# Kernel tuning notes

Measured on AMD Instinct MI355X. Metric: run time of the kernel, lower is better.

The kernel has to match this reference:

```python
import jax, jax.numpy as jnp
import numpy as np
import math

N = 100000          # nodes
E = 3200000         # edges
F_IN = 500          # num_features
HID = 64            # hidden
C = 64              # num_classes
K = 5               # trig frequencies
OMEGA = 1.0
D = 10              # Taylor order / diffusion hops


def _taylor_coeffs():
    # cos/sin Taylor coefficient tables, [K, D+1] (static, fp64 then cast)
    x = (np.arange(1, K + 1) * OMEGA * np.pi)[:, None].astype(np.float64)
    cosc = np.zeros((K, D + 1), np.float64)
    sinc = np.zeros((K, D + 1), np.float64)
    even = np.arange(0, D + 1, 2)
    cosc[:, ::2] = ((-1.0) ** (even // 2)) * x ** even / np.array([math.factorial(int(o)) for o in even], np.float64)
    odd = np.arange(1, D + 1, 2)
    sinc[:, 1::2] = ((-1.0) ** ((odd - 1) // 2)) * x ** odd / np.array([math.factorial(int(o)) for o in odd], np.float64)
    return jnp.asarray(sinc, jnp.float32), jnp.asarray(cosc, jnp.float32)

SINC, COSC = _taylor_coeffs()


def setup_inputs() -> dict:
    key = jax.random.key(0)
    ks = jax.random.split(key, 8)
    feature = jax.random.normal(ks[0], (N, F_IN), dtype=jnp.float32)
    edges = jax.random.randint(ks[1], (2, E), 0, N, dtype=jnp.int64)
    W1 = jax.random.normal(ks[2], (F_IN, HID), dtype=jnp.float32) * (1.0 / np.sqrt(F_IN))
    b1 = jnp.zeros((HID,), jnp.float32)
    W2 = jax.random.normal(ks[3], (HID, C), dtype=jnp.float32) * (1.0 / np.sqrt(HID))
    b2 = jnp.zeros((C,), jnp.float32)
    xav = np.sqrt(2.0 / (1 + K))  # xavier_normal for (1, K)
    alpha = jax.random.normal(ks[4], (1, K), dtype=jnp.float32) * xav
    beta = jax.random.normal(ks[5], (1, K), dtype=jnp.float32) * xav
    return {"feature": feature, "edges": edges, "W1": W1, "b1": b1,
            "W2": W2, "b2": b2, "alpha": alpha, "beta": beta}


def reference(feature, edges, W1, b1, W2, b2, alpha, beta):
    # dropout is identity in eval mode
    x = jnp.maximum(feature @ W1 + b1, 0.0)   # lin1 + relu
    x = x @ W2 + b2                           # lin2 -> [N, C]

    # ---- Trigo_prop.__norm__: sym-normalized Laplacian, rescale, self-loops -1 ----
    src, dst = edges[0], edges[1]
    not_loop = src != dst                     # remove_self_loops
    deg = jax.ops.segment_sum(jnp.where(not_loop, 1.0, 0.0).astype(x.dtype), src, num_segments=N)
    dinv = jnp.where(deg > 0, jax.lax.rsqrt(deg), 0.0)
    w_off = jnp.where(not_loop, -(dinv[src] * dinv[dst]), 0.0)   # off-diag of L_sym
    # Laplacian diagonal entries are all 1 -> lambda_max = 2*max(all weights)
    lam = 2.0 * jnp.maximum(jnp.max(w_off), 1.0)
    s = 2.0 / lam
    w_off = w_off * s
    diag = s * 1.0 - 1.0                      # scaled diag(1) plus appended -1 self-loop

    # ---- D-hop Taylor-weighted diffusion ----
    coeff = (alpha @ SINC + beta @ COSC)[0]   # [D+1]
    Tx = x
    hidden = coeff[0] * Tx
    for d in range(1, D + 1):                 # fixed small D, unrolled
        Tx = jax.ops.segment_sum(w_off[:, None] * Tx[src], dst, num_segments=N) + diag * Tx
        hidden = hidden + coeff[d] * Tx
    out = hidden + x
    return jax.nn.log_softmax(out, axis=1)
```

## Files before the change

### kernel.cpp

```cpp
#include <hip/hip_runtime.h>
#include <math.h>

#define NN 100000
#define FIN 500
#define HIDN 64
#define KF 5
#define DORD 10

typedef unsigned short ushort_t;

struct Tables { float sinc[KF][DORD+1]; float cosc[KF][DORD+1]; };

__device__ inline float bl(unsigned u) { return __uint_as_float(u << 16); }
__device__ inline float bh(unsigned u) { return __uint_as_float(u & 0xffff0000u); }
__device__ inline unsigned short bf16_rne(float x) {
    unsigned u = __float_as_uint(x);
    return (unsigned short)((u + 0x7fffu + ((u >> 16) & 1u)) >> 16);
}
__device__ inline unsigned pack_bf16x2(float a, float b) {
    return (unsigned)bf16_rne(a) | ((unsigned)bf16_rne(b) << 16);
}

__global__ void coeff_kernel(const float* __restrict__ alpha, const float* __restrict__ beta,
                             Tables tb, float* __restrict__ coeff) {
    int d = threadIdx.x;
    if (d <= DORD) {
        float c = 0.f;
        #pragma unroll
        for (int k = 0; k < KF; ++k)
            c += alpha[k] * tb.sinc[k][d] + beta[k] * tb.cosc[k][d];
        coeff[d] = c;
    }
}

#define CHUNK 8192
__global__ __launch_bounds__(256) void bin_hist_kernel(
    const int* __restrict__ src, const int* __restrict__ dst,
    int* __restrict__ deg, int* __restrict__ bucket_cnt,
    int E, int drng, int nb) {
    __shared__ int h[512];
    for (int i = threadIdx.x; i < nb; i += 256) h[i] = 0;
    __syncthreads();
    int base = blockIdx.x * CHUNK;
    int end = base + CHUNK; if (end > E) end = E;
    for (int e = base + threadIdx.x; e < end; e += 256) {
        int s = src[e], d = dst[e];
        if (s != d) {
            atomicAdd(&deg[s], 1);
            atomicAdd(&h[d / drng], 1);
        }
    }
    __syncthreads();
    for (int i = threadIdx.x; i < nb; i += 256)
        if (h[i]) atomicAdd(&bucket_cnt[i], h[i]);
}

__global__ void dinv_kernel(const int* __restrict__ deg, float* __restrict__ dinv, int n) {
    int i = blockIdx.x * blockDim.x + threadIdx.x;
    if (i >= n) return;
    int d = deg[i];
    dinv[i] = (d > 0) ? (1.0f / sqrtf((float)d)) : 0.f;
}

__global__ void bucket_scan_kernel(const int* __restrict__ bucket_cnt,
                                   int* __restrict__ bucket_off,
                                   int* __restrict__ bucket_cur, int nb) {
    __shared__ int tmp[512];
    int t = threadIdx.x;
    tmp[t] = (t < nb) ? bucket_cnt[t] : 0;
    __syncthreads();
    for (int off = 1; off < 512; off <<= 1) {
        int add = (t >= off) ? tmp[t - off] : 0;
        __syncthreads();
        tmp[t] += add;
        __syncthreads();
    }
    int excl = (t > 0) ? tmp[t - 1] : 0;
    if (t < nb) { bucket_off[t] = excl; bucket_cur[t] = excl; }
    if (t == nb - 1) bucket_off[nb] = tmp[t];
}

__global__ __launch_bounds__(256) void bin_scatter_kernel(
    const int* __restrict__ src, const int* __restrict__ dst,
    int* __restrict__ bucket_cur, uint2* __restrict__ binned,
    int E, int drng, int nb) {
    __shared__ int h[512];
    for (int i = threadIdx.x; i < nb; i += 256) h[i] = 0;
    __syncthreads();
    int base = blockIdx.x * CHUNK;
    int end = base + CHUNK; if (end > E) end = E;
    for (int e = base + threadIdx.x; e < end; e += 256) {
        int s = src[e], d = dst[e];
        if (s != d) atomicAdd(&h[d / drng], 1);
    }
    __syncthreads();
    for (int i = threadIdx.x; i < nb; i += 256) {
        int c = h[i];
        h[i] = c ? atomicAdd(&bucket_cur[i], c) : 0;
    }
    __syncthreads();
    for (int e = base + threadIdx.x; e < end; e += 256) {
        int s = src[e], d = dst[e];
        if (s != d) {
            int pos = atomicAdd(&h[d / drng], 1);
            binned[pos] = make_uint2((unsigned)s, (unsigned)d);
        }
    }
}

__global__ __launch_bounds__(256) void bucket_csr_kernel(
    const uint2* __restrict__ binned, const int* __restrict__ bucket_off,
    int* __restrict__ row_ptr, int* __restrict__ col,
    int n, int drng, int nb) {
    int b = blockIdx.x;
    int e0 = bucket_off[b], e1 = bucket_off[b + 1];
    int d0 = b * drng;
    int dn = n - d0; if (dn > drng) dn = drng;
    __shared__ int ind[256];
    __shared__ int cur[256];
    int t = threadIdx.x;
    ind[t] = 0;
    __syncthreads();
    for (int e = e0 + t; e < e1; e += 256) {
        uint2 p = binned[e];
        atomicAdd(&ind[(int)p.y - d0], 1);
    }
    __syncthreads();
    for (int off = 1; off < 256; off <<= 1) {
        int add = (t >= off) ? ind[t - off] : 0;
        __syncthreads();
        ind[t] += add;
        __syncthreads();
    }
    if (t < dn) {
        int excl = (t > 0) ? ind[t - 1] : 0;
        row_ptr[d0 + t] = e0 + excl;
        cur[t] = e0 + excl;
    }
    if (b == 0 && t == 0) row_ptr[n] = bucket_off[nb];
    __syncthreads();
    for (int e = e0 + t; e < e1; e += 256) {
        uint2 p = binned[e];
        int pos = atomicAdd(&cur[(int)p.y - d0], 1);
        col[pos] = (int)p.x;
    }
}

__global__ __launch_bounds__(256) void gemm1_kernel(
    const float* __restrict__ A, const float* __restrict__ W,
    const float* __restrict__ bias, float* __restrict__ H, int n) {
    __shared__ float sA[64][36];
    __shared__ float sW[32][64];
    int t = threadIdx.x;
    int tx = t & 15, ty = t >> 4;
    int rowBase = blockIdx.x * 64;
    float acc[4][4] = {{0.f}};
    for (int k0 = 0; k0 < FIN; k0 += 32) {
        #pragma unroll
        for (int l = 0; l < 2; ++l) {
            int c = t + l * 256;
            int r = c >> 3, cc = (c & 7) * 4;
            int gr = rowBase + r, gk = k0 + cc;
            float4 v = make_float4(0.f, 0.f, 0.f, 0.f);
            if (gr < n && gk < FIN) v = *(const float4*)(A + (size_t)gr * FIN + gk);
            *(float4*)&sA[r][cc] = v;
        }
        #pragma unroll
        for (int l = 0; l < 2; ++l) {
            int c = t + l * 256;
            int r = c >> 4, cc = (c & 15) * 4;
            int gk = k0 + r;
            float4 v = make_float4(0.f, 0.f, 0.f, 0.f);
            if (gk < FIN) v = *(const float4*)(W + (size_t)gk * 64 + cc);
            *(float4*)&sW[r][cc] = v;
        }
        __syncthreads();
        #pragma unroll
        for (int kk = 0; kk < 32; ++kk) {
            float a[4], b[4];
            #pragma unroll
            for (int i = 0; i < 4; ++i) a[i] = sA[ty * 4 + i][kk];
            #pragma unroll
            for (int j = 0; j < 4; ++j) b[j] = sW[kk][tx * 4 + j];
            #pragma unroll
            for (int i = 0; i < 4; ++i)
                #pragma unroll
                for (int j = 0; j < 4; ++j)
                    acc[i][j] = fmaf(a[i], b[j], acc[i][j]);
        }
        __syncthreads();
    }
    #pragma unroll
    for (int i = 0; i < 4; ++i) {
        int gr = rowBase + ty * 4 + i;
        if (gr < n) {
            float4 o;
            o.x = fmaxf(acc[i][0] + bias[tx * 4 + 0], 0.f);
            o.y = fmaxf(acc[i][1] + bias[tx * 4 + 1], 0.f);
            o.z = fmaxf(acc[i][2] + bias[tx * 4 + 2], 0.f);
            o.w = fmaxf(acc[i][3] + bias[tx * 4 + 3], 0.f);
            *(float4*)(H + (size_t)gr * 64 + tx * 4) = o;
        }
    }
}

__global__ __launch_bounds__(256) void gemm2_kernel(
    const float* __restrict__ H, const float* __restrict__ W2,
    const float* __restrict__ b2, const float* __restrict__ coeff,
    const float* __restrict__ dinv, ushort_t* __restrict__ ty0,
    float* __restrict__ out, int n) {
    __shared__ float sW[64 * 64];
    __shared__ float sb[64];
    int t = threadIdx.x;
    for (int i = t; i < 4096; i += 256) sW[i] = W2[i];
    if (t < 64) sb[t] = b2[t];
    __syncthreads();
    float c0p1 = 1.f + coeff[0];
    int lane = t & 63;
    int wid = t >> 6;
    int r0 = blockIdx.x * 128;
    int rend = r0 + 128; if (rend > n) rend = n;
    for (int r = r0 + wid; r < rend; r += 4) {
        float hv = H[(size_t)r * 64 + lane];
        float dr = dinv[r];
        float acc = sb[lane];
        #pragma unroll
        for (int k = 0; k < 64; ++k)
            acc = fmaf(__shfl(hv, k, 64), sW[k * 64 + lane], acc);
        ty0[(size_t)r * 64 + lane] = bf16_rne(dr * acc);
        out[(size_t)r * 64 + lane] = c0p1 * acc;
    }
}

__global__ __launch_bounds__(256) void spmm_kernel(
    const int* __restrict__ row_ptr, const int* __restrict__ col,
    const float* __restrict__ dinv, const ushort_t* __restrict__ tyin,
    ushort_t* __restrict__ tyout, float* __restrict__ out,
    const float* __restrict__ coeff, int d, int n, int fuse_lsm) {
    int wave = (blockIdx.x * blockDim.x + threadIdx.x) >> 6;
    if (wave >= n) return;
    int lane = threadIdx.x & 63;
    int sub = lane >> 4;
    int fl = lane & 15;
    int e0 = row_ptr[wave], e1 = row_ptr[wave + 1];
    float ax = 0.f, ay = 0.f, az = 0.f, aw = 0.f;
    int e = e0 + sub;
    for (; e + 12 < e1; e += 16) {
        int s0 = col[e], s1 = col[e + 4], s2 = col[e + 8], s3 = col[e + 12];
        uint2 p0 = *(const uint2*)(tyin + (size_t)s0 * 64 + fl * 4);
        uint2 p1 = *(const uint2*)(tyin + (size_t)s1 * 64 + fl * 4);
        uint2 p2 = *(const uint2*)(tyin + (size_t)s2 * 64 + fl * 4);
        uint2 p3 = *(const uint2*)(tyin + (size_t)s3 * 64 + fl * 4);
        ax += (bl(p0.x) + bl(p1.x)) + (bl(p2.x) + bl(p3.x));
        ay += (bh(p0.x) + bh(p1.x)) + (bh(p2.x) + bh(p3.x));
        az += (bl(p0.y) + bl(p1.y)) + (bl(p2.y) + bl(p3.y));
        aw += (bh(p0.y) + bh(p1.y)) + (bh(p2.y) + bh(p3.y));
    }
    for (; e < e1; e += 4) {
        int s = col[e];
        uint2 p = *(const uint2*)(tyin + (size_t)s * 64 + fl * 4);
        ax += bl(p.x); ay += bh(p.x); az += bl(p.y); aw += bh(p.y);
    }
    #pragma unroll
    for (int off = 16; off <= 32; off <<= 1) {
        ax += __shfl_xor(ax, off, 64);
        ay += __shfl_xor(ay, off, 64);
        az += __shfl_xor(az, off, 64);
        aw += __shfl_xor(aw, off, 64);
    }
    float dr = dinv[wave];
    float cd = coeff[d];
    float tx_x = -dr * ax, tx_y = -dr * ay, tx_z = -dr * az, tx_w = -dr * aw;
    float4 o = *(const float4*)(out + (size_t)wave * 64 + fl * 4);
    o.x += cd * tx_x; o.y += cd * tx_y; o.z += cd * tx_z; o.w += cd * tx_w;
    if (!fuse_lsm) {
        if (sub == 0) {
            uint2 ty;
            ty.x = pack_bf16x2(dr * tx_x, dr * tx_y);
            ty.y = pack_bf16x2(dr * tx_z, dr * tx_w);
            *(uint2*)(tyout + (size_t)wave * 64 + fl * 4) = ty;
            *(float4*)(out + (size_t)wave * 64 + fl * 4) = o;
        }
    } else {
        float m = fmaxf(fmaxf(o.x, o.y), fmaxf(o.z, o.w));
        #pragma unroll
        for (int off = 1; off < 16; off <<= 1) m = fmaxf(m, __shfl_xor(m, off, 64));
        float s4 = expf(o.x - m) + expf(o.y - m) + expf(o.z - m) + expf(o.w - m);
        #pragma unroll
        for (int off = 1; off < 16; off <<= 1) s4 += __shfl_xor(s4, off, 64);
        float lse = m + logf(s4);
        o.x -= lse; o.y -= lse; o.z -= lse; o.w -= lse;
        if (sub == 0)
            *(float4*)(out + (size_t)wave * 64 + fl * 4) = o;
    }
}

extern "C" void kernel_launch(void* const* d_in, const int* in_sizes, int n_in,
                              void* d_out, int out_size, void* d_ws, size_t ws_size,
                              hipStream_t stream) {
    const float* feature = (const float*)d_in[0];
    const int*   edges   = (const int*)d_in[1];
    const float* W1      = (const float*)d_in[2];
    const float* b1      = (const float*)d_in[3];
    const float* W2      = (const float*)d_in[4];
    const float* b2      = (const float*)d_in[5];
    const float* alpha   = (const float*)d_in[6];
    const float* beta    = (const float*)d_in[7];
    float* out = (float*)d_out;

    const int n = in_sizes[0] / FIN;
    const int E = in_sizes[1] / 2;
    const int* src = edges;
    const int* dst = edges + E;

    const int drng = (n + 511) / 512;
    const int nb   = (n + drng - 1) / drng;

    char* ws = (char*)d_ws;
    size_t off = 0;
    auto alloc = [&](size_t bytes) { size_t o = off; off = (off + bytes + 255) & ~(size_t)255; return o; };
    float*    coeff      = (float*)   (ws + alloc(64 * 4));
    int*      deg        = (int*)     (ws + alloc((size_t)n * 4));
    float*    dinv       = (float*)   (ws + alloc((size_t)n * 4));
    int*      row_ptr    = (int*)     (ws + alloc(((size_t)n + 1) * 4));
    int*      bucket_cnt = (int*)     (ws + alloc(512 * 4));
    int*      bucket_off = (int*)     (ws + alloc(513 * 4));
    int*      bucket_cur = (int*)     (ws + alloc(512 * 4));
    int*      col        = (int*)     (ws + alloc((size_t)E * 4));
    uint2*    binned     = (uint2*)   (ws + alloc((size_t)E * 8));
    float*    H          = (float*)   (ws + alloc((size_t)n * 64 * 4));
    ushort_t* TyA        = (ushort_t*)(ws + alloc((size_t)n * 64 * 2));
    ushort_t* TyB        = (ushort_t*)(ws + alloc((size_t)n * 64 * 2));

    Tables tb;
    for (int k = 0; k < KF; ++k) {
        double x = M_PI * (double)(k + 1);
        double p = 1.0, f = 1.0;
        for (int o = 0; o <= DORD; ++o) {
            if (o > 0) { p *= x; f *= (double)o; }
            double v = p / f;
            tb.cosc[k][o] = (o % 2 == 0) ? (float)((((o / 2) % 2 == 0) ? 1.0 : -1.0) * v) : 0.f;
            tb.sinc[k][o] = (o % 2 == 1) ? (float)(((((o - 1) / 2) % 2 == 0) ? 1.0 : -1.0) * v) : 0.f;
        }
    }

    hipMemsetAsync(deg, 0, (size_t)n * 4, stream);
    hipMemsetAsync(bucket_cnt, 0, 512 * 4, stream);

    coeff_kernel<<<1, 64, 0, stream>>>(alpha, beta, tb, coeff);

    int nchunk = (E + CHUNK - 1) / CHUNK;
    bin_hist_kernel<<<nchunk, 256, 0, stream>>>(src, dst, deg, bucket_cnt, E, drng, nb);
    dinv_kernel<<<(n + 255) / 256, 256, 0, stream>>>(deg, dinv, n);
    bucket_scan_kernel<<<1, 512, 0, stream>>>(bucket_cnt, bucket_off, bucket_cur, nb);
    bin_scatter_kernel<<<nchunk, 256, 0, stream>>>(src, dst, bucket_cur, binned, E, drng, nb);
    bucket_csr_kernel<<<nb, 256, 0, stream>>>(binned, bucket_off, row_ptr, col, n, drng, nb);

    gemm1_kernel<<<(n + 63) / 64, 256, 0, stream>>>(feature, W1, b1, H, n);
    gemm2_kernel<<<(n + 127) / 128, 256, 0, stream>>>(H, W2, b2, coeff, dinv, TyA, out, n);

    const ushort_t* tin = TyA;
    ushort_t* bufs[2] = { TyB, TyA };
    for (int d = 1; d <= DORD; ++d) {
        ushort_t* tout = bufs[(d - 1) & 1];
        spmm_kernel<<<(n + 3) / 4, 256, 0, stream>>>(row_ptr, col, dinv, tin, tout, out,
                                                     coeff, d, n, d == DORD ? 1 : 0);
        tin = tout;
    }
}
```

Before: 1.353 ms.

## Split bf16 features into column chunks for cache-resident SpMM gathers

Stores the propagated bf16 features as four separate 16-column slabs, each [n][16], and launches the SpMM over chunk-major blocks. Each pass then gathers from a 3.2MB slab that can stay in cache instead of the full 12.8MB matrix. Log-softmax moves into its own kernel. Degree counting is spread over 8 replicated counters to cut atomic contention, and CHUNK is halved. The cost is that each edge's col index is read four times and there are more blocks and launches.

```diff
diff --git a/kernel.cpp b/kernel.cpp
--- a/kernel.cpp
+++ b/kernel.cpp
@@ -6,6 +6,7 @@
 #define HIDN 64
 #define KF 5
 #define DORD 10
+#define CHUNK 4096
 
 typedef unsigned short ushort_t;
 
@@ -33,20 +34,20 @@
     }
 }
 
-#define CHUNK 8192
 __global__ __launch_bounds__(256) void bin_hist_kernel(
     const int* __restrict__ src, const int* __restrict__ dst,
-    int* __restrict__ deg, int* __restrict__ bucket_cnt,
-    int E, int drng, int nb) {
+    int* __restrict__ deg8, int* __restrict__ bucket_cnt,
+    int E, int drng, int nb, int n) {
     __shared__ int h[512];
     for (int i = threadIdx.x; i < nb; i += 256) h[i] = 0;
     __syncthreads();
+    int* degc = deg8 + (size_t)(blockIdx.x & 7) * n;
     int base = blockIdx.x * CHUNK;
     int end = base + CHUNK; if (end > E) end = E;
     for (int e = base + threadIdx.x; e < end; e += 256) {
         int s = src[e], d = dst[e];
         if (s != d) {
-            atomicAdd(&deg[s], 1);
+            atomicAdd(&degc[s], 1);
             atomicAdd(&h[d / drng], 1);
         }
     }
@@ -55,10 +56,12 @@
         if (h[i]) atomicAdd(&bucket_cnt[i], h[i]);
 }
 
-__global__ void dinv_kernel(const int* __restrict__ deg, float* __restrict__ dinv, int n) {
+__global__ void dinv_kernel(const int* __restrict__ deg8, float* __restrict__ dinv, int n) {
     int i = blockIdx.x * blockDim.x + threadIdx.x;
     if (i >= n) return;
-    int d = deg[i];
+    int d = 0;
+    #pragma unroll
+    for (int k = 0; k < 8; ++k) d += deg8[(size_t)k * n + i];
     dinv[i] = (d > 0) ? (1.0f / sqrtf((float)d)) : 0.f;
 }
 
@@ -207,7 +210,7 @@
 __global__ __launch_bounds__(256) void gemm2_kernel(
     const float* __restrict__ H, const float* __restrict__ W2,
     const float* __restrict__ b2, const float* __restrict__ coeff,
-    const float* __restrict__ dinv, ushort_t* __restrict__ ty0,
+    const float* __restrict__ dinv, unsigned* __restrict__ ty0,
     float* __restrict__ out, int n) {
     __shared__ float sW[64 * 64];
     __shared__ float sb[64];
@@ -227,72 +230,73 @@
         #pragma unroll
         for (int k = 0; k < 64; ++k)
             acc = fmaf(__shfl(hv, k, 64), sW[k * 64 + lane], acc);
-        ty0[(size_t)r * 64 + lane] = bf16_rne(dr * acc);
         out[(size_t)r * 64 + lane] = c0p1 * acc;
+        float accn = __shfl_xor(acc, 1, 64);
+        if (!(lane & 1)) {
+            int c = lane >> 4;
+            int fj = (lane & 15) >> 1;
+            ty0[((size_t)c * n + r) * 8 + fj] = pack_bf16x2(dr * acc, dr * accn);
+        }
     }
 }
 
 __global__ __launch_bounds__(256) void spmm_kernel(
     const int* __restrict__ row_ptr, const int* __restrict__ col,
-    const float* __restrict__ dinv, const ushort_t* __restrict__ tyin,
-    ushort_t* __restrict__ tyout, float* __restrict__ out,
-    const float* __restrict__ coeff, int d, int n, int fuse_lsm) {
+    const float* __restrict__ dinv, const unsigned* __restrict__ tyin,
+    unsigned* __restrict__ tyout, float* __restrict__ out,
+    const float* __restrict__ coeff, int d, int n, int bpc, int last) {
+    int blk = blockIdx.x;
+    int c = blk / bpc;
+    int r = (blk - c * bpc) * 4 + (threadIdx.x >> 6);
+    if (r >= n) return;
+    int lane = threadIdx.x & 63;
+    int sub = lane >> 3;
+    int fj = lane & 7;
+    const unsigned* tyc = tyin + (size_t)c * n * 8;
+    int e0 = row_ptr[r], e1 = row_ptr[r + 1];
+    float a0 = 0.f, a1 = 0.f;
+    int e = e0 + sub;
+    for (; e + 8 < e1; e += 16) {
+        unsigned p0 = tyc[((size_t)col[e] << 3) + fj];
+        unsigned p1 = tyc[((size_t)col[e + 8] << 3) + fj];
+        a0 += bl(p0) + bl(p1);
+        a1 += bh(p0) + bh(p1);
+    }
+    if (e < e1) {
+        unsigned p = tyc[((size_t)col[e] << 3) + fj];
+        a0 += bl(p); a1 += bh(p);
+    }
+    #pragma unroll
+    for (int off = 8; off <= 32; off <<= 1) {
+        a0 += __shfl_xor(a0, off, 64);
+        a1 += __shfl_xor(a1, off, 64);
+    }
+    if (sub == 0) {
+        float dr = dinv[r];
+        float cd = coeff[d];
+        float t0 = -dr * a0, t1 = -dr * a1;
+        float* op = out + (size_t)r * 64 + c * 16 + (fj << 1);
+        float2 o = *(float2*)op;
+        o.x += cd * t0; o.y += cd * t1;
+        *(float2*)op = o;
+        if (!last)
+            tyout[((size_t)c * n + r) * 8 + fj] = pack_bf16x2(dr * t0, dr * t1);
+    }
+}
+
+__global__ __launch_bounds__(256) void lsm_kernel(float* __restrict__ out, int n) {
     int wave = (blockIdx.x * blockDim.x + threadIdx.x) >> 6;
+    int lane = threadIdx.x & 63;
     if (wave >= n) return;
-    int lane = threadIdx.x & 63;
-    int sub = lane >> 4;
-    int fl = lane & 15;
-    int e0 = row_ptr[wave], e1 = row_ptr[wave + 1];
-    float ax = 0.f, ay = 0.f, az = 0.f, aw = 0.f;
-    int e = e0 + sub;
-    for (; e + 12 < e1; e += 16) {
-        int s0 = col[e], s1 = col[e + 4], s2 = col[e + 8], s3 = col[e + 12];
-        uint2 p0 = *(const uint2*)(tyin + (size_t)s0 * 64 + fl * 4);
-        uint2 p1 = *(const uint2*)(tyin + (size_t)s1 * 64 + fl * 4);
-        uint2 p2 = *(const uint2*)(tyin + (size_t)s2 * 64 + fl * 4);
-        uint2 p3 = *(const uint2*)(tyin + (size_t)s3 * 64 + fl * 4);
-        ax += (bl(p0.x) + bl(p1.x)) + (bl(p2.x) + bl(p3.x));
-        ay += (bh(p0.x) + bh(p1.x)) + (bh(p2.x) + bh(p3.x));
-        az += (bl(p0.y) + bl(p1.y)) + (bl(p2.y) + bl(p3.y));
-        aw += (bh(p0.y) + bh(p1.y)) + (bh(p2.y) + bh(p3.y));
-    }
-    for (; e < e1; e += 4) {
-        int s = col[e];
-        uint2 p = *(const uint2*)(tyin + (size_t)s * 64 + fl * 4);
-        ax += bl(p.x); ay += bh(p.x); az += bl(p.y); aw += bh(p.y);
-    }
-    #pragma unroll
-    for (int off = 16; off <= 32; off <<= 1) {
-        ax += __shfl_xor(ax, off, 64);
-        ay += __shfl_xor(ay, off, 64);
-        az += __shfl_xor(az, off, 64);
-        aw += __shfl_xor(aw, off, 64);
-    }
-    float dr = dinv[wave];
-    float cd = coeff[d];
-    float tx_x = -dr * ax, tx_y = -dr * ay, tx_z = -dr * az, tx_w = -dr * aw;
-    float4 o = *(const float4*)(out + (size_t)wave * 64 + fl * 4);
-    o.x += cd * tx_x; o.y += cd * tx_y; o.z += cd * tx_z; o.w += cd * tx_w;
-    if (!fuse_lsm) {
-        if (sub == 0) {
-            uint2 ty;
-            ty.x = pack_bf16x2(dr * tx_x, dr * tx_y);
-            ty.y = pack_bf16x2(dr * tx_z, dr * tx_w);
-            *(uint2*)(tyout + (size_t)wave * 64 + fl * 4) = ty;
-            *(float4*)(out + (size_t)wave * 64 + fl * 4) = o;
-        }
-    } else {
-        float m = fmaxf(fmaxf(o.x, o.y), fmaxf(o.z, o.w));
-        #pragma unroll
-        for (int off = 1; off < 16; off <<= 1) m = fmaxf(m, __shfl_xor(m, off, 64));
-        float s4 = expf(o.x - m) + expf(o.y - m) + expf(o.z - m) + expf(o.w - m);
-        #pragma unroll
-        for (int off = 1; off < 16; off <<= 1) s4 += __shfl_xor(s4, off, 64);
-        float lse = m + logf(s4);
-        o.x -= lse; o.y -= lse; o.z -= lse; o.w -= lse;
-        if (sub == 0)
-            *(float4*)(out + (size_t)wave * 64 + fl * 4) = o;
-    }
+    float v = out[(size_t)wave * 64 + lane];
+    float m = v;
+    #pragma unroll
+    for (int o = 32; o; o >>= 1) m = fmaxf(m, __shfl_xor(m, o, 64));
+    float ex = expf(v - m);
+    float ssum = ex;
+    #pragma unroll
+    for (int o = 32; o; o >>= 1) ssum += __shfl_xor(ssum, o, 64);
+    out[(size_t)wave * 64 + lane] = v - m - logf(ssum);
 }
 
 extern "C" void kernel_launch(void* const* d_in, const int* in_sizes, int n_in,
@@ -320,7 +324,7 @@
     size_t off = 0;
     auto alloc = [&](size_t bytes) { size_t o = off; off = (off + bytes + 255) & ~(size_t)255; return o; };
     float*    coeff      = (float*)   (ws + alloc(64 * 4));
-    int*      deg        = (int*)     (ws + alloc((size_t)n * 4));
+    int*      deg8       = (int*)     (ws + alloc((size_t)n * 8 * 4));
     float*    dinv       = (float*)   (ws + alloc((size_t)n * 4));
     int*      row_ptr    = (int*)     (ws + alloc(((size_t)n + 1) * 4));
     int*      bucket_cnt = (int*)     (ws + alloc(512 * 4));
@@ -329,8 +333,8 @@
     int*      col        = (int*)     (ws + alloc((size_t)E * 4));
     uint2*    binned     = (uint2*)   (ws + alloc((size_t)E * 8));
     float*    H          = (float*)   (ws + alloc((size_t)n * 64 * 4));
-    ushort_t* TyA        = (ushort_t*)(ws + alloc((size_t)n * 64 * 2));
-    ushort_t* TyB        = (ushort_t*)(ws + alloc((size_t)n * 64 * 2));
+    unsigned* TyA        = (unsigned*)(ws + alloc((size_t)n * 32 * 4));
+    unsigned* TyB        = (unsigned*)(ws + alloc((size_t)n * 32 * 4));
 
     Tables tb;
     for (int k = 0; k < KF; ++k) {
@@ -344,14 +348,14 @@
         }
     }
 
-    hipMemsetAsync(deg, 0, (size_t)n * 4, stream);
+    hipMemsetAsync(deg8, 0, (size_t)n * 8 * 4, stream);
     hipMemsetAsync(bucket_cnt, 0, 512 * 4, stream);
 
     coeff_kernel<<<1, 64, 0, stream>>>(alpha, beta, tb, coeff);
 
     int nchunk = (E + CHUNK - 1) / CHUNK;
-    bin_hist_kernel<<<nchunk, 256, 0, stream>>>(src, dst, deg, bucket_cnt, E, drng, nb);
-    dinv_kernel<<<(n + 255) / 256, 256, 0, stream>>>(deg, dinv, n);
+    bin_hist_kernel<<<nchunk, 256, 0, stream>>>(src, dst, deg8, bucket_cnt, E, drng, nb, n);
+    dinv_kernel<<<(n + 255) / 256, 256, 0, stream>>>(deg8, dinv, n);
     bucket_scan_kernel<<<1, 512, 0, stream>>>(bucket_cnt, bucket_off, bucket_cur, nb);
     bin_scatter_kernel<<<nchunk, 256, 0, stream>>>(src, dst, bucket_cur, binned, E, drng, nb);
     bucket_csr_kernel<<<nb, 256, 0, stream>>>(binned, bucket_off, row_ptr, col, n, drng, nb);
@@ -359,12 +363,14 @@
     gemm1_kernel<<<(n + 63) / 64, 256, 0, stream>>>(feature, W1, b1, H, n);
     gemm2_kernel<<<(n + 127) / 128, 256, 0, stream>>>(H, W2, b2, coeff, dinv, TyA, out, n);
 
-    const ushort_t* tin = TyA;
-    ushort_t* bufs[2] = { TyB, TyA };
+    const int bpc = (n + 3) / 4;
+    const unsigned* tin = TyA;
+    unsigned* bufs[2] = { TyB, TyA };
     for (int d = 1; d <= DORD; ++d) {
-        ushort_t* tout = bufs[(d - 1) & 1];
-        spmm_kernel<<<(n + 3) / 4, 256, 0, stream>>>(row_ptr, col, dinv, tin, tout, out,
-                                                     coeff, d, n, d == DORD ? 1 : 0);
+        unsigned* tout = bufs[(d - 1) & 1];
+        spmm_kernel<<<bpc * 4, 256, 0, stream>>>(row_ptr, col, dinv, tin, tout, out,
+                                                 coeff, d, n, bpc, d == DORD ? 1 : 0);
         tin = tout;
     }
-}
+    lsm_kernel<<<(n + 3) / 4, 256, 0, stream>>>(out, n);
+}
```

New measurement: 2.310 ms. 70.8% more time.
